# Performance work log

Measured on AMD Instinct MI355X. Metric: run time of the kernel, lower is better.

## Reference

```python
import jax, jax.numpy as jnp
import numpy as np

EPS = 1e-5


def _layer_norm(x, gamma, beta):
    mu = jnp.mean(x, axis=-1, keepdims=True)
    var = jnp.var(x, axis=-1, keepdims=True)
    return (x - mu) * jax.lax.rsqrt(var + EPS) * gamma + beta


def setup_inputs() -> dict:
    key = jax.random.key(0)
    B, I, H = 4096, 1024, 1024
    ks = jax.random.split(key, 6)
    x = jax.random.normal(ks[0], (B, I), dtype=jnp.float32)
    h = jax.random.normal(ks[1], (B, H), dtype=jnp.float32)
    c = jax.random.normal(ks[2], (B, H), dtype=jnp.float32)
    # nn.Linear(I+H, 4H): weight [4H, I+H], bias [4H]
    bound = 1.0 / np.sqrt(I + H)
    W = jax.random.uniform(ks[3], (4 * H, I + H), minval=-bound, maxval=bound, dtype=jnp.float32)
    b = jax.random.uniform(ks[4], (4 * H,), minval=-bound, maxval=bound, dtype=jnp.float32)
    inp = {"x": x, "h": h, "c": c, "W": W, "b": b}
    for name in ("i", "f", "g", "o", "c"):
        inp[f"ln_{name}_g"] = jnp.ones((H,), dtype=jnp.float32)
        inp[f"ln_{name}_b"] = jnp.zeros((H,), dtype=jnp.float32)
    return inp


def reference(x, h, c, W, b, ln_i_g, ln_i_b, ln_f_g, ln_f_b, ln_g_g, ln_g_b,
              ln_o_g, ln_o_b, ln_c_g, ln_c_b):
    H = h.shape[-1]
    xh = jnp.concatenate([x, h], axis=-1)              # [B, I+H]
    gates = xh @ W.T + b                               # [B, 4H]
    i_raw, f_raw, g_raw, o_raw = jnp.split(gates, 4, axis=-1)
    i = jax.nn.sigmoid(_layer_norm(i_raw, ln_i_g, ln_i_b))
    f = jax.nn.sigmoid(_layer_norm(f_raw, ln_f_g, ln_f_b))
    g = jnp.tanh(_layer_norm(g_raw, ln_g_g, ln_g_b))
    o = jax.nn.sigmoid(_layer_norm(o_raw, ln_o_g, ln_o_b))
    c_new = f * c + i * g
    h_new = o * jnp.tanh(_layer_norm(c_new, ln_c_g, ln_c_b))
    return (h_new, c_new)
```

## Files before the change

### kernel.cpp

```cpp
#include <hip/hip_runtime.h>
#include <hip/hip_bf16.h>

#define B_ROWS 4096
#define H_DIM  1024
#define K_DIM  2048
#define N_DIM  4096
#define NT     32

typedef __attribute__((ext_vector_type(8))) short bf16x8;
typedef __attribute__((ext_vector_type(4))) float f32x4;

__device__ __forceinline__ unsigned short f2bf(float f) {
  union { float f; unsigned int u; } v; v.f = f;
  unsigned int u = v.u;
  return (unsigned short)((u + 0x7fffu + ((u >> 16) & 1u)) >> 16);
}
__device__ __forceinline__ float bf2f(unsigned short u) {
  union { unsigned int u; float f; } v; v.u = ((unsigned int)u) << 16;
  return v.f;
}

__device__ __forceinline__ void gload_lds16(const void* g, void* l) {
  __builtin_amdgcn_global_load_lds(
      (const __attribute__((address_space(1))) void*)g,
      (__attribute__((address_space(3))) void*)l, 16, 0, 0);
}

__global__ __launch_bounds__(256) void pack_kernel(
    const float* __restrict__ x, const float* __restrict__ h,
    const float* __restrict__ W, unsigned short* __restrict__ Abf,
    unsigned short* __restrict__ Wbf) {
  int bid = blockIdx.x;
  if (bid < 8192) {
    int t = bid * 256 + threadIdx.x;
    int e = t * 4;
    int row = e >> 11;
    int col = e & 2047;
    const float* src = (col < 1024) ? (x + (size_t)row * 1024 + col)
                                    : (h + (size_t)row * 1024 + (col - 1024));
    float4 v = *(const float4*)src;
    ushort4 o;
    o.x = f2bf(v.x); o.y = f2bf(v.y); o.z = f2bf(v.z); o.w = f2bf(v.w);
    *(ushort4*)(Abf + e) = o;
  } else {
    int t = (bid - 8192) * 256 + threadIdx.x;
    int e = t * 4;
    float4 v = *(const float4*)(W + e);
    ushort4 o;
    o.x = f2bf(v.x); o.y = f2bf(v.y); o.z = f2bf(v.z); o.w = f2bf(v.w);
    *(ushort4*)(Wbf + e) = o;
  }
}


#define STAGE(g, kt, dst) do {                              \
    gload_lds16((g) + (size_t)(kt) * 64, (dst));            \
    gload_lds16((g) + (size_t)(kt) * 64 + 32, (dst) + 1024); } while (0)

#define WAIT_LGKM0() do {                                   \
    asm volatile("s_waitcnt lgkmcnt(0)" ::: "memory");      \
    __builtin_amdgcn_sched_barrier(0); } while (0)

__global__ __launch_bounds__(512, 2) void gemm_kernel(
    const unsigned short* __restrict__ A, const unsigned short* __restrict__ W,
    const float* __restrict__ bias, unsigned short* __restrict__ C) {
  __shared__ __align__(16) char lds[131072];

  const int tid = threadIdx.x;
  const int w = tid >> 6, l = tid & 63;
  const int wm = w >> 2, wn = w & 3;
  const int bm = blockIdx.y * 256, bn = blockIdx.x * 256;

  const int lofs = (((l & 15) * 64) + ((l >> 4) * 16)) ^ ((l & 8) << 2);
  const int lane_r = (l >> 2) & 15;
  const int lane_c = ((l & 3) * 8) ^ (((l >> 5) & 1) * 16);

  const int rbA0 = w + (w & 4);
  const int rbA1 = rbA0 + 4;
  const int rbB0 = ((w >> 1) << 2) + (w & 1);
  const int rbB1 = rbB0 + 2;

  const unsigned short* gA0 = A + (size_t)(bm + rbA0 * 16 + lane_r) * K_DIM + lane_c;
  const unsigned short* gA1 = A + (size_t)(bm + rbA1 * 16 + lane_r) * K_DIM + lane_c;
  const unsigned short* gB0 = W + (size_t)(bn + rbB0 * 16 + lane_r) * K_DIM + lane_c;
  const unsigned short* gB1 = W + (size_t)(bn + rbB1 * 16 + lane_r) * K_DIM + lane_c;

  char* const L0 = lds;
  char* const L1 = lds + 65536;

  f32x4 acc[8][4];
#pragma unroll
  for (int i = 0; i < 8; ++i)
#pragma unroll
    for (int j = 0; j < 4; ++j) acc[i][j] = (f32x4)0.0f;

  STAGE(gA0, 0, L0 + rbA0 * 2048);
  STAGE(gB0, 0, L0 + 32768 + rbB0 * 2048);
  STAGE(gB1, 0, L0 + 32768 + rbB1 * 2048);
  STAGE(gA1, 0, L0 + rbA1 * 2048);
  STAGE(gA0, 1, L1 + rbA0 * 2048);
  STAGE(gB0, 1, L1 + 32768 + rbB0 * 2048);
  STAGE(gB1, 1, L1 + 32768 + rbB1 * 2048);
  asm volatile("s_waitcnt vmcnt(6)" ::: "memory");
  __builtin_amdgcn_s_barrier();

  bf16x8 a0[4][2], a1[4][2], b0[2][2], b1[2][2];

#pragma unroll
  for (int mi = 0; mi < 4; ++mi)
#pragma unroll
    for (int kk = 0; kk < 2; ++kk)
      a0[mi][kk] = *(const bf16x8*)(L0 + (((wm * 8 + mi) * 2 + kk) << 10) + lofs);
#pragma unroll
  for (int ni = 0; ni < 2; ++ni)
#pragma unroll
    for (int kk = 0; kk < 2; ++kk)
      b0[ni][kk] = *(const bf16x8*)(L0 + 32768 + (((wn * 4 + ni) * 2 + kk) << 10) + lofs);

#pragma unroll 2
  for (int t = 0; t < NT; ++t) {
    const int buf = t & 1;
    char* const Lc = lds + buf * 65536;
    char* const Ln = lds + (buf ^ 1) * 65536;
    const char* const LA = Lc;
    const char* const LB = Lc + 32768;
    const char* const LAn = Ln;
    const char* const LBn = Ln + 32768;
    const int kt1 = (t + 1) & (NT - 1);
    const int kt2 = (t + 2) & (NT - 1);

    STAGE(gA1, kt1, Ln + rbA1 * 2048);
    __builtin_amdgcn_s_barrier();
    WAIT_LGKM0();
    __builtin_amdgcn_s_setprio(1);
#pragma unroll
    for (int ni = 0; ni < 2; ++ni)
#pragma unroll
      for (int kk = 0; kk < 2; ++kk)
        b1[ni][kk] = *(const bf16x8*)(LB + (((wn * 4 + 2 + ni) * 2 + kk) << 10) + lofs);
#pragma unroll
    for (int mi = 0; mi < 4; ++mi)
#pragma unroll
      for (int ni = 0; ni < 2; ++ni)
#pragma unroll
        for (int kk = 0; kk < 2; ++kk)
          acc[mi][ni] = __builtin_amdgcn_mfma_f32_16x16x32_bf16(
              a0[mi][kk], b0[ni][kk], acc[mi][ni], 0, 0, 0);
    __builtin_amdgcn_s_setprio(0);
    __builtin_amdgcn_s_barrier();

    STAGE(gA0, kt2, Lc + rbA0 * 2048);
    __builtin_amdgcn_s_barrier();
    WAIT_LGKM0();
    __builtin_amdgcn_s_setprio(1);
#pragma unroll
    for (int mi = 0; mi < 4; ++mi)
#pragma unroll
      for (int kk = 0; kk < 2; ++kk)
        a1[mi][kk] = *(const bf16x8*)(LA + (((wm * 8 + 4 + mi) * 2 + kk) << 10) + lofs);
#pragma unroll
    for (int mi = 0; mi < 4; ++mi)
#pragma unroll
      for (int ni = 0; ni < 2; ++ni)
#pragma unroll
        for (int kk = 0; kk < 2; ++kk)
          acc[mi][2 + ni] = __builtin_amdgcn_mfma_f32_16x16x32_bf16(
              a0[mi][kk], b1[ni][kk], acc[mi][2 + ni], 0, 0, 0);
    __builtin_amdgcn_s_setprio(0);
    __builtin_amdgcn_s_barrier();

    STAGE(gB0, kt2, Lc + 32768 + rbB0 * 2048);
    __builtin_amdgcn_s_barrier();
    WAIT_LGKM0();
    __builtin_amdgcn_s_setprio(1);
#pragma unroll
    for (int mi = 0; mi < 4; ++mi)
#pragma unroll
      for (int ni = 0; ni < 2; ++ni)
#pragma unroll
        for (int kk = 0; kk < 2; ++kk)
          acc[4 + mi][2 + ni] = __builtin_amdgcn_mfma_f32_16x16x32_bf16(
              a1[mi][kk], b1[ni][kk], acc[4 + mi][2 + ni], 0, 0, 0);
    __builtin_amdgcn_s_setprio(0);
    __builtin_amdgcn_s_barrier();

    STAGE(gB1, kt2, Lc + 32768 + rbB1 * 2048);
    asm volatile("s_waitcnt vmcnt(6)" ::: "memory");
    __builtin_amdgcn_s_barrier();
    __builtin_amdgcn_s_setprio(1);
#pragma unroll
    for (int mi = 0; mi < 4; ++mi)
#pragma unroll
      for (int ni = 0; ni < 2; ++ni)
#pragma unroll
        for (int kk = 0; kk < 2; ++kk)
          acc[4 + mi][ni] = __builtin_amdgcn_mfma_f32_16x16x32_bf16(
              a1[mi][kk], b0[ni][kk], acc[4 + mi][ni], 0, 0, 0);
    __builtin_amdgcn_s_setprio(0);
#pragma unroll
    for (int mi = 0; mi < 4; ++mi)
#pragma unroll
      for (int kk = 0; kk < 2; ++kk)
        a0[mi][kk] = *(const bf16x8*)(LAn + (((wm * 8 + mi) * 2 + kk) << 10) + lofs);
#pragma unroll
    for (int ni = 0; ni < 2; ++ni)
#pragma unroll
      for (int kk = 0; kk < 2; ++kk)
        b0[ni][kk] = *(const bf16x8*)(LBn + (((wn * 4 + ni) * 2 + kk) << 10) + lofs);
    __builtin_amdgcn_s_barrier();
  }

  const int lm = l & 15, lq = l >> 4;
  float bv[4];
#pragma unroll
  for (int ni = 0; ni < 4; ++ni) bv[ni] = bias[bn + wn * 64 + ni * 16 + lm];
  unsigned short* Cb = C + (size_t)(bm + wm * 128) * N_DIM + bn + wn * 64;
#pragma unroll
  for (int mi = 0; mi < 8; ++mi)
#pragma unroll
    for (int j = 0; j < 4; ++j) {
      const size_t rofs = (size_t)(mi * 16 + lq * 4 + j) * N_DIM;
#pragma unroll
      for (int ni = 0; ni < 4; ++ni)
        Cb[rofs + ni * 16 + lm] = f2bf(acc[mi][ni][j] + bv[ni]);
    }
}

__device__ __forceinline__ float2 blk_sum2(float s, float q, float* red,
                                           int wid, int lane) {
#pragma unroll
  for (int o = 32; o >= 1; o >>= 1) {
    s += __shfl_xor(s, o, 64);
    q += __shfl_xor(q, o, 64);
  }
  __syncthreads();
  if (lane == 0) { red[wid * 2] = s; red[wid * 2 + 1] = q; }
  __syncthreads();
  s = red[0] + red[2] + red[4] + red[6];
  q = red[1] + red[3] + red[5] + red[7];
  return make_float2(s, q);
}

__device__ __forceinline__ float sigmoidf_(float x) {
  return 1.0f / (1.0f + __expf(-x));
}
__device__ __forceinline__ float tanhf_(float x) {
  return 1.0f - 2.0f / (__expf(2.0f * x) + 1.0f);
}

__global__ __launch_bounds__(256) void ln_lstm_kernel(
    const unsigned short* __restrict__ gates, const float* __restrict__ cprev,
    const float* __restrict__ g_i, const float* __restrict__ b_i,
    const float* __restrict__ g_f, const float* __restrict__ b_f,
    const float* __restrict__ g_g, const float* __restrict__ b_g,
    const float* __restrict__ g_o, const float* __restrict__ b_o,
    const float* __restrict__ g_c, const float* __restrict__ b_c,
    float* __restrict__ out) {
  const int b = blockIdx.x;
  const int t = threadIdx.x;
  const int wid = t >> 6, lane = t & 63;
  __shared__ float red[8];

  const unsigned short* grow = gates + (size_t)b * N_DIM;
  const int c0 = t * 4;

  float v[4][4];
#pragma unroll
  for (int g = 0; g < 4; g++) {
    ushort4 raw = *(const ushort4*)(grow + g * 1024 + c0);
    v[g][0] = bf2f(raw.x); v[g][1] = bf2f(raw.y);
    v[g][2] = bf2f(raw.z); v[g][3] = bf2f(raw.w);
  }

  const float4 gamma[4] = {*(const float4*)(g_i + c0), *(const float4*)(g_f + c0),
                           *(const float4*)(g_g + c0), *(const float4*)(g_o + c0)};
  const float4 beta[4]  = {*(const float4*)(b_i + c0), *(const float4*)(b_f + c0),
                           *(const float4*)(b_g + c0), *(const float4*)(b_o + c0)};

  float a[4][4];
#pragma unroll
  for (int g = 0; g < 4; g++) {
    float s = v[g][0] + v[g][1] + v[g][2] + v[g][3];
    float q = v[g][0]*v[g][0] + v[g][1]*v[g][1] + v[g][2]*v[g][2] + v[g][3]*v[g][3];
    float2 r = blk_sum2(s, q, red, wid, lane);
    float mu = r.x * (1.0f / 1024.0f);
    float var = r.y * (1.0f / 1024.0f) - mu * mu;
    float inv = rsqrtf(var + 1e-5f);
    const float* gm = (const float*)&gamma[g];
    const float* bt = (const float*)&beta[g];
#pragma unroll
    for (int j = 0; j < 4; j++) {
      float n = (v[g][j] - mu) * inv * gm[j] + bt[j];
      a[g][j] = (g == 2) ? tanhf_(n) : sigmoidf_(n);
    }
  }

  float4 cp = *(const float4*)(cprev + (size_t)b * 1024 + c0);
  const float* cpe = (const float*)&cp;
  float cn[4];
#pragma unroll
  for (int j = 0; j < 4; j++)
    cn[j] = a[1][j] * cpe[j] + a[0][j] * a[2][j];

  {
    float s = cn[0] + cn[1] + cn[2] + cn[3];
    float q = cn[0]*cn[0] + cn[1]*cn[1] + cn[2]*cn[2] + cn[3]*cn[3];
    float2 r = blk_sum2(s, q, red, wid, lane);
    float mu = r.x * (1.0f / 1024.0f);
    float var = r.y * (1.0f / 1024.0f) - mu * mu;
    float inv = rsqrtf(var + 1e-5f);
    float4 gm = *(const float4*)(g_c + c0);
    float4 bt = *(const float4*)(b_c + c0);
    const float* gme = (const float*)&gm;
    const float* bte = (const float*)&bt;
    float hn[4];
#pragma unroll
    for (int j = 0; j < 4; j++) {
      float n = (cn[j] - mu) * inv * gme[j] + bte[j];
      hn[j] = a[3][j] * tanhf_(n);
    }
    *(float4*)(out + (size_t)b * 1024 + c0) = make_float4(hn[0], hn[1], hn[2], hn[3]);
    *(float4*)(out + (size_t)B_ROWS * H_DIM + (size_t)b * 1024 + c0) =
        make_float4(cn[0], cn[1], cn[2], cn[3]);
  }
}

extern "C" void kernel_launch(void* const* d_in, const int* in_sizes, int n_in,
                              void* d_out, int out_size, void* d_ws,
                              size_t ws_size, hipStream_t stream) {
  const float* x    = (const float*)d_in[0];
  const float* h    = (const float*)d_in[1];
  const float* c    = (const float*)d_in[2];
  const float* W    = (const float*)d_in[3];
  const float* bias = (const float*)d_in[4];
  const float* ln_i_g = (const float*)d_in[5];
  const float* ln_i_b = (const float*)d_in[6];
  const float* ln_f_g = (const float*)d_in[7];
  const float* ln_f_b = (const float*)d_in[8];
  const float* ln_g_g = (const float*)d_in[9];
  const float* ln_g_b = (const float*)d_in[10];
  const float* ln_o_g = (const float*)d_in[11];
  const float* ln_o_b = (const float*)d_in[12];
  const float* ln_c_g = (const float*)d_in[13];
  const float* ln_c_b = (const float*)d_in[14];

  unsigned short* Abf = (unsigned short*)d_ws;
  unsigned short* Wbf = Abf + (size_t)B_ROWS * K_DIM;
  unsigned short* gates = Wbf + (size_t)N_DIM * K_DIM;

  pack_kernel<<<16384, 256, 0, stream>>>(x, h, W, Abf, Wbf);

  dim3 ggrid(N_DIM / 256, B_ROWS / 256);
  gemm_kernel<<<ggrid, 512, 0, stream>>>(Abf, Wbf, bias, gates);

  ln_lstm_kernel<<<B_ROWS, 256, 0, stream>>>(
      gates, c, ln_i_g, ln_i_b, ln_f_g, ln_f_b, ln_g_g, ln_g_b,
      ln_o_g, ln_o_b, ln_c_g, ln_c_b, (float*)d_out);
}
```

Before: 102.8 us.

## Double-buffer B0 fragments across tiles and remap blocks per XCD for L2 locality

```diff
diff --git a/kernel.cpp b/kernel.cpp
--- a/kernel.cpp
+++ b/kernel.cpp
@@ -61,6 +61,80 @@
     asm volatile("s_waitcnt lgkmcnt(0)" ::: "memory");      \
     __builtin_amdgcn_sched_barrier(0); } while (0)
 
+#define UNR _Pragma("unroll")
+
+#define TILE(tt, BUF, B0R, B0W)                                              \
+  {                                                                          \
+    char* const Lc = lds + (BUF) * 65536;                                    \
+    char* const Ln = lds + ((BUF) ^ 1) * 65536;                              \
+    const int kt1 = ((tt) + 1) & (NT - 1);                                   \
+    const int kt2 = ((tt) + 2) & (NT - 1);                                   \
+        \
+    STAGE(gA1, kt1, Ln + rbA1 * 2048);                                       \
+    __builtin_amdgcn_s_barrier();                                            \
+    WAIT_LGKM0();                                                            \
+    __builtin_amdgcn_s_setprio(1);                                           \
+    UNR for (int ni = 0; ni < 2; ++ni)                                       \
+      UNR for (int kk = 0; kk < 2; ++kk)                                     \
+        b1[ni][kk] = *(const bf16x8*)(Lc + 32768 +                           \
+            (((wn * 4 + 2 + ni) * 2 + kk) << 10) + lofs);                    \
+    UNR for (int mi = 0; mi < 4; ++mi)                                       \
+      UNR for (int ni = 0; ni < 2; ++ni)                                     \
+        UNR for (int kk = 0; kk < 2; ++kk)                                   \
+          acc[mi][ni] = __builtin_amdgcn_mfma_f32_16x16x32_bf16(             \
+              a0[mi][kk], B0R[ni][kk], acc[mi][ni], 0, 0, 0);                \
+    __builtin_amdgcn_s_setprio(0);                                           \
+    __builtin_amdgcn_s_barrier();                                            \
+         \
+    STAGE(gA0, kt2, Lc + rbA0 * 2048);                                       \
+    __builtin_amdgcn_s_barrier();                                            \
+    WAIT_LGKM0();                                                            \
+    __builtin_amdgcn_s_setprio(1);                                           \
+    UNR for (int mi = 0; mi < 4; ++mi)                                       \
+      UNR for (int kk = 0; kk < 2; ++kk)                                     \
+        a1[mi][kk] = *(const bf16x8*)(Lc +                                   \
+            (((wm * 8 + 4 + mi) * 2 + kk) << 10) + lofs);                    \
+    UNR for (int mi = 0; mi < 4; ++mi)                                       \
+      UNR for (int ni = 0; ni < 2; ++ni)                                     \
+        UNR for (int kk = 0; kk < 2; ++kk)                                   \
+          acc[mi][2 + ni] = __builtin_amdgcn_mfma_f32_16x16x32_bf16(         \
+              a0[mi][kk], b1[ni][kk], acc[mi][2 + ni], 0, 0, 0);             \
+    __builtin_amdgcn_s_setprio(0);                                           \
+    __builtin_amdgcn_s_barrier();                                            \
+                  \
+    STAGE(gB0, kt2, Lc + 32768 + rbB0 * 2048);                               \
+    __builtin_amdgcn_s_barrier();                                            \
+    WAIT_LGKM0();                                                            \
+    __builtin_amdgcn_s_setprio(1);                                           \
+    UNR for (int mi = 0; mi < 4; ++mi)                                       \
+      UNR for (int ni = 0; ni < 2; ++ni)                                     \
+        UNR for (int kk = 0; kk < 2; ++kk)                                   \
+          acc[4 + mi][2 + ni] = __builtin_amdgcn_mfma_f32_16x16x32_bf16(     \
+              a1[mi][kk], b1[ni][kk], acc[4 + mi][2 + ni], 0, 0, 0);         \
+    __builtin_amdgcn_s_setprio(0);                                           \
+    __builtin_amdgcn_s_barrier();                                            \
+          \
+    STAGE(gB1, kt2, Lc + 32768 + rbB1 * 2048);                               \
+    asm volatile("s_waitcnt vmcnt(6)" ::: "memory");                         \
+    __builtin_amdgcn_s_barrier();                                            \
+    __builtin_amdgcn_s_setprio(1);                                           \
+    UNR for (int mi = 0; mi < 4; ++mi)                                       \
+      UNR for (int kk = 0; kk < 2; ++kk)                                     \
+        a0[mi][kk] = *(const bf16x8*)(Ln +                                   \
+            (((wm * 8 + mi) * 2 + kk) << 10) + lofs);                        \
+    UNR for (int ni = 0; ni < 2; ++ni)                                       \
+      UNR for (int kk = 0; kk < 2; ++kk)                                     \
+        B0W[ni][kk] = *(const bf16x8*)(Ln + 32768 +                          \
+            (((wn * 4 + ni) * 2 + kk) << 10) + lofs);                        \
+    UNR for (int mi = 0; mi < 4; ++mi)                                       \
+      UNR for (int ni = 0; ni < 2; ++ni)                                     \
+        UNR for (int kk = 0; kk < 2; ++kk)                                   \
+          acc[4 + mi][ni] = __builtin_amdgcn_mfma_f32_16x16x32_bf16(         \
+              a1[mi][kk], B0R[ni][kk], acc[4 + mi][ni], 0, 0, 0);            \
+    __builtin_amdgcn_s_setprio(0);                                           \
+    __builtin_amdgcn_s_barrier();                                            \
+  }
+
 __global__ __launch_bounds__(512, 2) void gemm_kernel(
     const unsigned short* __restrict__ A, const unsigned short* __restrict__ W,
     const float* __restrict__ bias, unsigned short* __restrict__ C) {
@@ -69,7 +143,12 @@
   const int tid = threadIdx.x;
   const int w = tid >> 6, l = tid & 63;
   const int wm = w >> 2, wn = w & 3;
-  const int bm = blockIdx.y * 256, bn = blockIdx.x * 256;
+
+  const int bid = blockIdx.x;
+  const int xcd = bid & 7, li = bid >> 3;
+  const int by = (xcd & 3) * 4 + (li >> 3);
+  const int bx = ((xcd >> 2) << 3) + (li & 7);
+  const int bm = by * 256, bn = bx * 256;
 
   const int lofs = (((l & 15) * 64) + ((l >> 4) * 16)) ^ ((l & 8) << 2);
   const int lane_r = (l >> 2) & 15;
@@ -95,16 +174,16 @@
     for (int j = 0; j < 4; ++j) acc[i][j] = (f32x4)0.0f;
 
   STAGE(gA0, 0, L0 + rbA0 * 2048);
+  STAGE(gA1, 0, L0 + rbA1 * 2048);
   STAGE(gB0, 0, L0 + 32768 + rbB0 * 2048);
   STAGE(gB1, 0, L0 + 32768 + rbB1 * 2048);
-  STAGE(gA1, 0, L0 + rbA1 * 2048);
   STAGE(gA0, 1, L1 + rbA0 * 2048);
   STAGE(gB0, 1, L1 + 32768 + rbB0 * 2048);
   STAGE(gB1, 1, L1 + 32768 + rbB1 * 2048);
   asm volatile("s_waitcnt vmcnt(6)" ::: "memory");
   __builtin_amdgcn_s_barrier();
 
-  bf16x8 a0[4][2], a1[4][2], b0[2][2], b1[2][2];
+  bf16x8 a0[4][2], a1[4][2], b0P[2][2], b0Q[2][2], b1[2][2];
 
 #pragma unroll
   for (int mi = 0; mi < 4; ++mi)
@@ -115,99 +194,11 @@
   for (int ni = 0; ni < 2; ++ni)
 #pragma unroll
     for (int kk = 0; kk < 2; ++kk)
-      b0[ni][kk] = *(const bf16x8*)(L0 + 32768 + (((wn * 4 + ni) * 2 + kk) << 10) + lofs);
-
-#pragma unroll 2
-  for (int t = 0; t < NT; ++t) {
-    const int buf = t & 1;
-    char* const Lc = lds + buf * 65536;
-    char* const Ln = lds + (buf ^ 1) * 65536;
-    const char* const LA = Lc;
-    const char* const LB = Lc + 32768;
-    const char* const LAn = Ln;
-    const char* const LBn = Ln + 32768;
-    const int kt1 = (t + 1) & (NT - 1);
-    const int kt2 = (t + 2) & (NT - 1);
-
-    STAGE(gA1, kt1, Ln + rbA1 * 2048);
-    __builtin_amdgcn_s_barrier();
-    WAIT_LGKM0();
-    __builtin_amdgcn_s_setprio(1);
-#pragma unroll
-    for (int ni = 0; ni < 2; ++ni)
-#pragma unroll
-      for (int kk = 0; kk < 2; ++kk)
-        b1[ni][kk] = *(const bf16x8*)(LB + (((wn * 4 + 2 + ni) * 2 + kk) << 10) + lofs);
-#pragma unroll
-    for (int mi = 0; mi < 4; ++mi)
-#pragma unroll
-      for (int ni = 0; ni < 2; ++ni)
-#pragma unroll
-        for (int kk = 0; kk < 2; ++kk)
-          acc[mi][ni] = __builtin_amdgcn_mfma_f32_16x16x32_bf16(
-              a0[mi][kk], b0[ni][kk], acc[mi][ni], 0, 0, 0);
-    __builtin_amdgcn_s_setprio(0);
-    __builtin_amdgcn_s_barrier();
-
-    STAGE(gA0, kt2, Lc + rbA0 * 2048);
-    __builtin_amdgcn_s_barrier();
-    WAIT_LGKM0();
-    __builtin_amdgcn_s_setprio(1);
-#pragma unroll
-    for (int mi = 0; mi < 4; ++mi)
-#pragma unroll
-      for (int kk = 0; kk < 2; ++kk)
-        a1[mi][kk] = *(const bf16x8*)(LA + (((wm * 8 + 4 + mi) * 2 + kk) << 10) + lofs);
-#pragma unroll
-    for (int mi = 0; mi < 4; ++mi)
-#pragma unroll
-      for (int ni = 0; ni < 2; ++ni)
-#pragma unroll
-        for (int kk = 0; kk < 2; ++kk)
-          acc[mi][2 + ni] = __builtin_amdgcn_mfma_f32_16x16x32_bf16(
-              a0[mi][kk], b1[ni][kk], acc[mi][2 + ni], 0, 0, 0);
-    __builtin_amdgcn_s_setprio(0);
-    __builtin_amdgcn_s_barrier();
-
-    STAGE(gB0, kt2, Lc + 32768 + rbB0 * 2048);
-    __builtin_amdgcn_s_barrier();
-    WAIT_LGKM0();
-    __builtin_amdgcn_s_setprio(1);
-#pragma unroll
-    for (int mi = 0; mi < 4; ++mi)
-#pragma unroll
-      for (int ni = 0; ni < 2; ++ni)
-#pragma unroll
-        for (int kk = 0; kk < 2; ++kk)
-          acc[4 + mi][2 + ni] = __builtin_amdgcn_mfma_f32_16x16x32_bf16(
-              a1[mi][kk], b1[ni][kk], acc[4 + mi][2 + ni], 0, 0, 0);
-    __builtin_amdgcn_s_setprio(0);
-    __builtin_amdgcn_s_barrier();
-
-    STAGE(gB1, kt2, Lc + 32768 + rbB1 * 2048);
-    asm volatile("s_waitcnt vmcnt(6)" ::: "memory");
-    __builtin_amdgcn_s_barrier();
-    __builtin_amdgcn_s_setprio(1);
-#pragma unroll
-    for (int mi = 0; mi < 4; ++mi)
-#pragma unroll
-      for (int ni = 0; ni < 2; ++ni)
-#pragma unroll
-        for (int kk = 0; kk < 2; ++kk)
-          acc[4 + mi][ni] = __builtin_amdgcn_mfma_f32_16x16x32_bf16(
-              a1[mi][kk], b0[ni][kk], acc[4 + mi][ni], 0, 0, 0);
-    __builtin_amdgcn_s_setprio(0);
-#pragma unroll
-    for (int mi = 0; mi < 4; ++mi)
-#pragma unroll
-      for (int kk = 0; kk < 2; ++kk)
-        a0[mi][kk] = *(const bf16x8*)(LAn + (((wm * 8 + mi) * 2 + kk) << 10) + lofs);
-#pragma unroll
-    for (int ni = 0; ni < 2; ++ni)
-#pragma unroll
-      for (int kk = 0; kk < 2; ++kk)
-        b0[ni][kk] = *(const bf16x8*)(LBn + (((wn * 4 + ni) * 2 + kk) << 10) + lofs);
-    __builtin_amdgcn_s_barrier();
+      b0P[ni][kk] = *(const bf16x8*)(L0 + 32768 + (((wn * 4 + ni) * 2 + kk) << 10) + lofs);
+
+  for (int t = 0; t < NT; t += 2) {
+    TILE(t, 0, b0P, b0Q);
+    TILE(t + 1, 1, b0Q, b0P);
   }
 
   const int lm = l & 15, lq = l >> 4;
@@ -350,7 +341,7 @@
 
   pack_kernel<<<16384, 256, 0, stream>>>(x, h, W, Abf, Wbf);
 
-  dim3 ggrid(N_DIM / 256, B_ROWS / 256);
+  dim3 ggrid(256);
   gemm_kernel<<<ggrid, 512, 0, stream>>>(Abf, Wbf, bias, gates);
 
   ln_lstm_kernel<<<B_ROWS, 256, 0, stream>>>(
```

After: 102.3 us. About the same (-0.5%).
